# Optimization experiments

Hardware: AMD Instinct MI355X
Metric: run time of the kernel (lower is better)

Reference implementation:

```python
import jax, jax.numpy as jnp
import numpy as np

ENC_H = 512
DEC_H = 1024

def setup_inputs() -> dict:
    key = jax.random.key(0)
    k1, k2, k3, k4 = jax.random.split(key, 4)
    B, S = 32, 2048
    s = jax.random.normal(k1, (B, DEC_H), dtype=jnp.float32)
    encoder_outputs = jax.random.normal(k2, (B, S, 2 * ENC_H), dtype=jnp.float32)
    # nn.Linear weights: attn: [dec_h, 2*enc_h + dec_h], v: [1, dec_h]
    fan_in_attn = 2 * ENC_H + DEC_H
    attn_w = jax.random.uniform(k3, (DEC_H, fan_in_attn), dtype=jnp.float32,
                                minval=-1.0, maxval=1.0) / np.sqrt(fan_in_attn)
    v_w = jax.random.uniform(k4, (1, DEC_H), dtype=jnp.float32,
                             minval=-1.0, maxval=1.0) / np.sqrt(DEC_H)
    return {"s": s, "encoder_outputs": encoder_outputs, "attn_w": attn_w, "v_w": v_w}

def reference(s, encoder_outputs, attn_w, v_w):
    # Split attn weight to avoid materializing the repeated/concatenated tensor:
    # cat([s_rep, enc], -1) @ W^T == s @ Ws^T (broadcast over S) + enc @ We^T
    W_s = attn_w[:, :DEC_H]            # [dec_h, dec_h] acts on s
    W_e = attn_w[:, DEC_H:]            # [dec_h, 2*enc_h] acts on encoder_outputs
    proj_s = jnp.einsum('bd,hd->bh', s, W_s)                   # [B, dec_h]
    proj_e = jnp.einsum('bse,he->bsh', encoder_outputs, W_e)   # [B, S, dec_h]
    energy = jnp.tanh(proj_s[:, None, :] + proj_e)             # [B, S, dec_h]
    scores = jnp.einsum('bsh,oh->bs', energy, v_w)             # [B, S]
    return jax.nn.softmax(scores, axis=1)
```

## Files before the change

kernel.cpp:

```cpp
#include <hip/hip_runtime.h>
#include <hip/hip_bf16.h>

#define KDIM 1024
#define HDIM 1024
#define BM   64

typedef __attribute__((ext_vector_type(8))) short bf16x8_t;
typedef __attribute__((ext_vector_type(16))) float f32x16_t;
typedef __attribute__((ext_vector_type(4))) float f32x4_t;
typedef __attribute__((ext_vector_type(4))) unsigned int u32x4_t;
typedef __attribute__((ext_vector_type(2))) unsigned int u32x2_t;

__device__ __forceinline__ unsigned int pack2bf(float a, float b) {
    union { float f; unsigned int u; } ua, ub;
    ua.f = a; ub.f = b;
    unsigned int ra = (ua.u + 0x7fffu + ((ua.u >> 16) & 1u)) >> 16;
    unsigned int rb = (ub.u + 0x7fffu + ((ub.u >> 16) & 1u)) >> 16;
    return ra | (rb << 16);
}

__global__ void cvt_we_k(const float* __restrict__ attn_w, unsigned short* __restrict__ we_t) {
    const int h = blockIdx.x;
    const int t = threadIdx.x;
    const f32x4_t v = *(const f32x4_t*)(attn_w + (size_t)h * 2048 + 1024 + (size_t)t * 4);
    u32x2_t o;
    o[0] = pack2bf(v[0], v[1]);
    o[1] = pack2bf(v[2], v[3]);
    const int ks  = t >> 2;
    const int e15 = (t & 3) * 4;
    *(u32x2_t*)&we_t[(size_t)ks * 16384 + h * 16 + e15] = o;
}

__global__ void proj_s_k(const float* __restrict__ s, const float* __restrict__ attn_w,
                         float* __restrict__ ps) {
    const int h = (blockIdx.x * blockDim.x + threadIdx.x) >> 6;
    const int lane = threadIdx.x & 63;
    const float* wr = attn_w + (size_t)h * 2048;
    float w[16];
#pragma unroll
    for (int i = 0; i < 16; ++i) w[i] = wr[lane + 64 * i];
    for (int b = 0; b < 32; ++b) {
        const float* sr = s + (size_t)b * 1024;
        float a = 0.f;
#pragma unroll
        for (int i = 0; i < 16; ++i) a = fmaf(w[i], sr[lane + 64 * i], a);
#pragma unroll
        for (int off = 32; off >= 1; off >>= 1) a += __shfl_xor(a, off, 64);
        if (lane == 0) ps[b * 1024 + h] = a;
    }
}

__launch_bounds__(512, 2)
__global__ void fused_main_k(const float* __restrict__ enc,
                             const unsigned short* __restrict__ we_t,
                             const float* __restrict__ ps,
                             const float* __restrict__ vw,
                             float* __restrict__ scores) {
    __shared__ unsigned short lds_a[4 * 64 * 128];

    const int t = threadIdx.x;
    const int bid = blockIdx.x;
    const int swz = (bid & 7) * 128 + (bid >> 3);
    const int m_base = swz * BM;
    const int bidx = swz >> 5;

    const int lane = t & 63;
    const int wid  = t >> 6;
    const int l31  = lane & 31;
    const int h5   = lane >> 5;
    const int hb   = wid * 128;

    const int srow = t >> 4;
    const int sc8  = t & 15;

    auto stage_load = [&](int kc, f32x4_t* r) {
#pragma unroll
        for (int i = 0; i < 2; ++i) {
            const int row = i * 32 + srow;
            const float* p = enc + (size_t)(m_base + row) * KDIM + kc * 128 + sc8 * 8;
            r[2 * i]     = __builtin_nontemporal_load((const f32x4_t*)p);
            r[2 * i + 1] = __builtin_nontemporal_load((const f32x4_t*)(p + 4));
        }
    };
    auto stage_write = [&](int kc, const f32x4_t* r) {
        const int slot = kc & 3;
#pragma unroll
        for (int i = 0; i < 2; ++i) {
            const int row = i * 32 + srow;
            u32x4_t p;
            p[0] = pack2bf(r[2 * i][0], r[2 * i][1]);
            p[1] = pack2bf(r[2 * i][2], r[2 * i][3]);
            p[2] = pack2bf(r[2 * i + 1][0], r[2 * i + 1][1]);
            p[3] = pack2bf(r[2 * i + 1][2], r[2 * i + 1][3]);
            *(u32x4_t*)&lds_a[slot * 8192 + row * 128 + ((sc8 ^ (row & 7)) << 3)] = p;
        }
    };

    const unsigned short* btile = we_t + (size_t)(hb + l31) * 16 + h5 * 8;
    auto loadB = [&](int g, bf16x8_t* dst) {
        const unsigned short* bp = btile + (size_t)g * 16384;
        dst[0] = *(const bf16x8_t*)(bp);
        dst[1] = *(const bf16x8_t*)(bp + 512);
        dst[2] = *(const bf16x8_t*)(bp + 1024);
        dst[3] = *(const bf16x8_t*)(bp + 1536);
    };

    f32x16_t acc[2][4];
#pragma unroll
    for (int m = 0; m < 2; ++m)
#pragma unroll
        for (int nf = 0; nf < 4; ++nf)
#pragma unroll
            for (int r = 0; r < 16; ++r) acc[m][nf][r] = 0.f;

    bf16x8_t bbuf[4][4];

    loadB(0, bbuf[0]);
    loadB(1, bbuf[1]);
    loadB(2, bbuf[2]);
    {
        f32x4_t r0[4], r1[4];
        stage_load(0, r0);
        stage_load(1, r1);
        stage_write(0, r0);
        stage_write(1, r1);
    }
    __syncthreads();

    const int xr = h5 ^ (l31 & 7);
    const int a0base = l31 * 128;
    const int a1base = (32 + l31) * 128;

    f32x4_t rs[4];
#pragma unroll
    for (int g = 0; g < 64; ++g) {
        const int kc  = g >> 3;
        const int ksl = g & 7;

        if (g + 3 < 64) loadB(g + 3, bbuf[(g + 3) & 3]);
        if (ksl == 3 && kc < 6) stage_load(kc + 2, rs);

        const unsigned short* slotp = lds_a + (kc & 3) * 8192;
        const int coff = ((ksl * 2) ^ xr) << 3;
        const bf16x8_t a0 = *(const bf16x8_t*)&slotp[a0base + coff];
        const bf16x8_t a1 = *(const bf16x8_t*)&slotp[a1base + coff];
        const bf16x8_t* bfr = bbuf[g & 3];
#pragma unroll
        for (int nf = 0; nf < 4; ++nf) {
            acc[0][nf] = __builtin_amdgcn_mfma_f32_32x32x16_bf16(a0, bfr[nf], acc[0][nf], 0, 0, 0);
            acc[1][nf] = __builtin_amdgcn_mfma_f32_32x32x16_bf16(a1, bfr[nf], acc[1][nf], 0, 0, 0);
        }
        if (ksl == 7) {
            if (kc < 6) stage_write(kc + 2, rs);
            __syncthreads();
        }
    }

    float sc2[2][16];
#pragma unroll
    for (int m = 0; m < 2; ++m)
#pragma unroll
        for (int r = 0; r < 16; ++r) sc2[m][r] = 0.f;

#pragma unroll
    for (int nf = 0; nf < 4; ++nf) {
        const int h = hb + nf * 32 + l31;
        const float pv = ps[bidx * 1024 + h];
        const float vv = vw[h];
#pragma unroll
        for (int m = 0; m < 2; ++m)
#pragma unroll
            for (int r = 0; r < 16; ++r) {
                const float x = acc[m][nf][r] + pv;
                const float e = __expf(2.0f * x);
                const float th = 1.0f - __fdividef(2.0f, e + 1.0f);
                sc2[m][r] = fmaf(vv, th, sc2[m][r]);
            }
    }

#pragma unroll
    for (int off = 1; off < 32; off <<= 1)
#pragma unroll
        for (int m = 0; m < 2; ++m)
#pragma unroll
            for (int r = 0; r < 16; ++r)
                sc2[m][r] += __shfl_xor(sc2[m][r], off, 64);

    __syncthreads();
    float* slds = (float*)lds_a;
    if (l31 == 0) {
#pragma unroll
        for (int m = 0; m < 2; ++m)
#pragma unroll
            for (int r = 0; r < 16; ++r) {
                const int row = m * 32 + (r & 3) + 8 * (r >> 2) + 4 * h5;
                slds[wid * 64 + row] = sc2[m][r];
            }
    }
    __syncthreads();
    if (t < 64) {
        float v = 0.f;
#pragma unroll
        for (int w = 0; w < 8; ++w) v += slds[w * 64 + t];
        scores[m_base + t] = v;
    }
}

__global__ void softmax_k(const float* __restrict__ sc, float* __restrict__ out) {
    const int b = blockIdx.x;
    const int t = threadIdx.x;
    const int lane = t & 63;
    const int w = t >> 6;
    const float* row = sc + (size_t)b * 2048;
    float x[8];
#pragma unroll
    for (int i = 0; i < 8; ++i) x[i] = row[i * 256 + t];
    float m = x[0];
#pragma unroll
    for (int i = 1; i < 8; ++i) m = fmaxf(m, x[i]);
#pragma unroll
    for (int off = 32; off >= 1; off >>= 1) m = fmaxf(m, __shfl_xor(m, off, 64));
    __shared__ float sred[4];
    __shared__ float sred2[4];
    if (lane == 0) sred[w] = m;
    __syncthreads();
    m = fmaxf(fmaxf(sred[0], sred[1]), fmaxf(sred[2], sred[3]));
    float ssum = 0.f;
#pragma unroll
    for (int i = 0; i < 8; ++i) { x[i] = expf(x[i] - m); ssum += x[i]; }
#pragma unroll
    for (int off = 32; off >= 1; off >>= 1) ssum += __shfl_xor(ssum, off, 64);
    if (lane == 0) sred2[w] = ssum;
    __syncthreads();
    const float inv = 1.0f / (sred2[0] + sred2[1] + sred2[2] + sred2[3]);
#pragma unroll
    for (int i = 0; i < 8; ++i) out[(size_t)b * 2048 + i * 256 + t] = x[i] * inv;
}

extern "C" void kernel_launch(void* const* d_in, const int* in_sizes, int n_in,
                              void* d_out, int out_size, void* d_ws, size_t ws_size,
                              hipStream_t stream) {
    const float* s      = (const float*)d_in[0];
    const float* enc    = (const float*)d_in[1];
    const float* attn_w = (const float*)d_in[2];
    const float* vw     = (const float*)d_in[3];
    float* out = (float*)d_out;

    unsigned short* we = (unsigned short*)d_ws;
    float* ps     = (float*)((char*)d_ws + (2u << 20));
    float* scores = (float*)((char*)d_ws + (2u << 20) + (128u << 10));

    cvt_we_k<<<1024, 256, 0, stream>>>(attn_w, we);
    proj_s_k<<<256, 256, 0, stream>>>(s, attn_w, ps);
    fused_main_k<<<1024, 512, 0, stream>>>(enc, we, ps, vw, scores);
    softmax_k<<<32, 256, 0, stream>>>(scores, out);
}
```

Measured before the change: 223.5 us.

## Split hidden dimension across two blocks and halve LDS staging for occupancy

The main GEMM kernel now launches twice as many blocks, each handling half of the hidden dimension (512 columns), and writes partial scores that the softmax kernel sums. Per-block accumulators, B fragments and the LDS ring (now double-buffered instead of 4 slots) shrink, so launch bounds allow 4 blocks per CU. The aim is more occupancy and latency hiding. The cost is that each encoder tile is read and converted twice, doubling the dominant HBM traffic unless L2 catches the reuse.

```diff
diff --git a/kernel.cpp b/kernel.cpp
--- a/kernel.cpp
+++ b/kernel.cpp
@@ -4,6 +4,7 @@
 #define KDIM 1024
 #define HDIM 1024
 #define BM   64
+#define SPART 65536
 
 typedef __attribute__((ext_vector_type(8))) short bf16x8_t;
 typedef __attribute__((ext_vector_type(16))) float f32x16_t;
@@ -50,108 +51,96 @@
     }
 }
 
-__launch_bounds__(512, 2)
+__launch_bounds__(512, 4)
 __global__ void fused_main_k(const float* __restrict__ enc,
                              const unsigned short* __restrict__ we_t,
                              const float* __restrict__ ps,
                              const float* __restrict__ vw,
-                             float* __restrict__ scores) {
-    __shared__ unsigned short lds_a[4 * 64 * 128];
+                             float* __restrict__ scores_part) {
+    __shared__ unsigned short lds_a[2 * 64 * 128];
 
     const int t = threadIdx.x;
     const int bid = blockIdx.x;
-    const int swz = (bid & 7) * 128 + (bid >> 3);
-    const int m_base = swz * BM;
-    const int bidx = swz >> 5;
+    const int m_swz = (bid & 7) * 128 + ((bid >> 3) & 127);
+    const int hhalf = bid >> 10;
+    const int m_base = m_swz * BM;
+    const int bidx = m_swz >> 5;
 
     const int lane = t & 63;
     const int wid  = t >> 6;
     const int l31  = lane & 31;
     const int h5   = lane >> 5;
-    const int hb   = wid * 128;
+    const int habs = hhalf * 512 + wid * 64;
 
     const int srow = t >> 4;
     const int sc8  = t & 15;
 
-    auto stage_load = [&](int kc, f32x4_t* r) {
-#pragma unroll
-        for (int i = 0; i < 2; ++i) {
-            const int row = i * 32 + srow;
-            const float* p = enc + (size_t)(m_base + row) * KDIM + kc * 128 + sc8 * 8;
-            r[2 * i]     = __builtin_nontemporal_load((const f32x4_t*)p);
-            r[2 * i + 1] = __builtin_nontemporal_load((const f32x4_t*)(p + 4));
-        }
+    auto stage_load_half = [&](int kc, int half, f32x4_t* r) {
+        const int row = half * 32 + srow;
+        const float* p = enc + (size_t)(m_base + row) * KDIM + kc * 128 + sc8 * 8;
+        r[0] = __builtin_nontemporal_load((const f32x4_t*)p);
+        r[1] = __builtin_nontemporal_load((const f32x4_t*)(p + 4));
     };
-    auto stage_write = [&](int kc, const f32x4_t* r) {
-        const int slot = kc & 3;
-#pragma unroll
-        for (int i = 0; i < 2; ++i) {
-            const int row = i * 32 + srow;
-            u32x4_t p;
-            p[0] = pack2bf(r[2 * i][0], r[2 * i][1]);
-            p[1] = pack2bf(r[2 * i][2], r[2 * i][3]);
-            p[2] = pack2bf(r[2 * i + 1][0], r[2 * i + 1][1]);
-            p[3] = pack2bf(r[2 * i + 1][2], r[2 * i + 1][3]);
-            *(u32x4_t*)&lds_a[slot * 8192 + row * 128 + ((sc8 ^ (row & 7)) << 3)] = p;
-        }
+    auto stage_write_half = [&](int kc, int half, const f32x4_t* r) {
+        const int slot = kc & 1;
+        const int row = half * 32 + srow;
+        u32x4_t pk;
+        pk[0] = pack2bf(r[0][0], r[0][1]);
+        pk[1] = pack2bf(r[0][2], r[0][3]);
+        pk[2] = pack2bf(r[1][0], r[1][1]);
+        pk[3] = pack2bf(r[1][2], r[1][3]);
+        *(u32x4_t*)&lds_a[slot * 8192 + row * 128 + ((sc8 ^ (row & 15)) << 3)] = pk;
     };
 
-    const unsigned short* btile = we_t + (size_t)(hb + l31) * 16 + h5 * 8;
+    const unsigned short* btile = we_t + (size_t)(habs + l31) * 16 + h5 * 8;
     auto loadB = [&](int g, bf16x8_t* dst) {
         const unsigned short* bp = btile + (size_t)g * 16384;
         dst[0] = *(const bf16x8_t*)(bp);
         dst[1] = *(const bf16x8_t*)(bp + 512);
-        dst[2] = *(const bf16x8_t*)(bp + 1024);
-        dst[3] = *(const bf16x8_t*)(bp + 1536);
     };
 
-    f32x16_t acc[2][4];
+    f32x16_t acc[2][2];
 #pragma unroll
     for (int m = 0; m < 2; ++m)
 #pragma unroll
-        for (int nf = 0; nf < 4; ++nf)
+        for (int nf = 0; nf < 2; ++nf)
 #pragma unroll
             for (int r = 0; r < 16; ++r) acc[m][nf][r] = 0.f;
 
-    bf16x8_t bbuf[4][4];
+    bf16x8_t bbuf[4][2];
+    f32x4_t rsA[2], rsB[2];
 
     loadB(0, bbuf[0]);
     loadB(1, bbuf[1]);
     loadB(2, bbuf[2]);
-    {
-        f32x4_t r0[4], r1[4];
-        stage_load(0, r0);
-        stage_load(1, r1);
-        stage_write(0, r0);
-        stage_write(1, r1);
-    }
-    __syncthreads();
-
-    const int xr = h5 ^ (l31 & 7);
-    const int a0base = l31 * 128;
-    const int a1base = (32 + l31) * 128;
-
-    f32x4_t rs[4];
+    stage_load_half(0, 0, rsA);
+    stage_load_half(0, 1, rsB);
+    stage_write_half(0, 0, rsA);
+    stage_write_half(0, 1, rsB);
+    __syncthreads();
+
 #pragma unroll
     for (int g = 0; g < 64; ++g) {
         const int kc  = g >> 3;
         const int ksl = g & 7;
 
         if (g + 3 < 64) loadB(g + 3, bbuf[(g + 3) & 3]);
-        if (ksl == 3 && kc < 6) stage_load(kc + 2, rs);
-
-        const unsigned short* slotp = lds_a + (kc & 3) * 8192;
-        const int coff = ((ksl * 2) ^ xr) << 3;
-        const bf16x8_t a0 = *(const bf16x8_t*)&slotp[a0base + coff];
-        const bf16x8_t a1 = *(const bf16x8_t*)&slotp[a1base + coff];
+        if (ksl == 0 && kc < 7) stage_load_half(kc + 1, 0, rsA);
+        if (ksl == 4 && kc < 7) stage_load_half(kc + 1, 1, rsB);
+
+        const unsigned short* slotp = lds_a + (kc & 1) * 8192;
+        const int ch = (((ksl << 1) + h5) ^ (l31 & 15)) << 3;
+        const bf16x8_t a0 = *(const bf16x8_t*)&slotp[l31 * 128 + ch];
+        const bf16x8_t a1 = *(const bf16x8_t*)&slotp[(32 + l31) * 128 + ch];
         const bf16x8_t* bfr = bbuf[g & 3];
-#pragma unroll
-        for (int nf = 0; nf < 4; ++nf) {
-            acc[0][nf] = __builtin_amdgcn_mfma_f32_32x32x16_bf16(a0, bfr[nf], acc[0][nf], 0, 0, 0);
-            acc[1][nf] = __builtin_amdgcn_mfma_f32_32x32x16_bf16(a1, bfr[nf], acc[1][nf], 0, 0, 0);
-        }
+        acc[0][0] = __builtin_amdgcn_mfma_f32_32x32x16_bf16(a0, bfr[0], acc[0][0], 0, 0, 0);
+        acc[1][0] = __builtin_amdgcn_mfma_f32_32x32x16_bf16(a1, bfr[0], acc[1][0], 0, 0, 0);
+        acc[0][1] = __builtin_amdgcn_mfma_f32_32x32x16_bf16(a0, bfr[1], acc[0][1], 0, 0, 0);
+        acc[1][1] = __builtin_amdgcn_mfma_f32_32x32x16_bf16(a1, bfr[1], acc[1][1], 0, 0, 0);
+
+        if (ksl == 3 && kc < 7) stage_write_half(kc + 1, 0, rsA);
         if (ksl == 7) {
-            if (kc < 6) stage_write(kc + 2, rs);
+            if (kc < 7) stage_write_half(kc + 1, 1, rsB);
             __syncthreads();
         }
     }
@@ -163,8 +152,8 @@
         for (int r = 0; r < 16; ++r) sc2[m][r] = 0.f;
 
 #pragma unroll
-    for (int nf = 0; nf < 4; ++nf) {
-        const int h = hb + nf * 32 + l31;
+    for (int nf = 0; nf < 2; ++nf) {
+        const int h = habs + nf * 32 + l31;
         const float pv = ps[bidx * 1024 + h];
         const float vv = vw[h];
 #pragma unroll
@@ -202,7 +191,7 @@
         float v = 0.f;
 #pragma unroll
         for (int w = 0; w < 8; ++w) v += slds[w * 64 + t];
-        scores[m_base + t] = v;
+        scores_part[(size_t)hhalf * SPART + m_base + t] = v;
     }
 }
 
@@ -211,10 +200,11 @@
     const int t = threadIdx.x;
     const int lane = t & 63;
     const int w = t >> 6;
-    const float* row = sc + (size_t)b * 2048;
+    const float* r0 = sc + (size_t)b * 2048;
+    const float* r1 = sc + SPART + (size_t)b * 2048;
     float x[8];
 #pragma unroll
-    for (int i = 0; i < 8; ++i) x[i] = row[i * 256 + t];
+    for (int i = 0; i < 8; ++i) x[i] = r0[i * 256 + t] + r1[i * 256 + t];
     float m = x[0];
 #pragma unroll
     for (int i = 1; i < 8; ++i) m = fmaxf(m, x[i]);
@@ -252,6 +242,6 @@
 
     cvt_we_k<<<1024, 256, 0, stream>>>(attn_w, we);
     proj_s_k<<<256, 256, 0, stream>>>(s, attn_w, ps);
-    fused_main_k<<<1024, 512, 0, stream>>>(enc, we, ps, vw, scores);
+    fused_main_k<<<2048, 512, 0, stream>>>(enc, we, ps, vw, scores);
     softmax_k<<<32, 256, 0, stream>>>(scores, out);
 }
```

Result: slower. 237.4 us (+6.2%).
